# Performance work log

Hardware: AMD Instinct MI355X
Metric: run time of the kernel (lower is better)

The kernel has to match this reference:

```python
import jax, jax.numpy as jnp
import numpy as np
from jax import lax

DIM = 1024
H = 16          # num_heads
HD = DIM // H   # head dim (qk and v identical)
D_INNER = 4     # fast-weight inner dim
CHUNK = 16
BASE_LR = 1e-3
KSZ = 4         # short conv kernel size


def short_conv(x, w):
    # x: (b, l, c), w: (c, KSZ). Depthwise causal conv + residual (as in ShortConvolution).
    xT = jnp.transpose(x, (0, 2, 1))  # (b, c, l)
    y = lax.conv_general_dilated(xT, w[:, None, :], window_strides=(1,),
                                 padding=[(KSZ - 1, 0)], feature_group_count=x.shape[-1],
                                 dimension_numbers=('NCH', 'OIH', 'NCH'))
    return jnp.transpose(y + xT, (0, 2, 1))


def l2norm(x):
    # interpret torch.norm(..., dim=-1) as L2 normalization over head dim (required for shape consistency)
    return x / jnp.linalg.norm(x, axis=-1, keepdims=True)


def attn(q, k, v):
    # flash_attn_func equivalent: non-causal softmax attention, scale 1/sqrt(d)
    # q: (b, D, h, d), k/v: (b, L, h, d)
    s = jnp.einsum('bqhd,bkhd->bhqk', q, k) / jnp.sqrt(jnp.asarray(q.shape[-1], q.dtype))
    p = jax.nn.softmax(s, axis=-1)
    return jnp.einsum('bhqk,bkhd->bqhd', p, v)


def setup_inputs() -> dict:
    key = jax.random.key(0)
    ks = jax.random.split(key, 12)
    b, l = 4, 4096
    s = 1.0 / np.sqrt(DIM)
    return {
        'hidden_states': jax.random.normal(ks[0], (b, l, DIM), jnp.float32),
        'Wq': jax.random.normal(ks[1], (DIM, DIM), jnp.float32) * s,
        'Wk': jax.random.normal(ks[2], (DIM, DIM), jnp.float32) * s,
        'Wv': jax.random.normal(ks[3], (DIM, DIM), jnp.float32) * s,
        'Wlr': jax.random.normal(ks[4], (H * 2, DIM), jnp.float32) * s,
        'Wg': jax.random.normal(ks[5], (DIM, DIM), jnp.float32) * s,
        'Wo': jax.random.normal(ks[6], (DIM, DIM), jnp.float32) * s,
        'cq': jax.random.normal(ks[7], (DIM, KSZ), jnp.float32) * 0.1,
        'ck': jax.random.normal(ks[8], (DIM, KSZ), jnp.float32) * 0.1,
        'cv': jax.random.normal(ks[9], (DIM, KSZ), jnp.float32) * 0.1,
        'W_in_init': jax.random.normal(ks[10], (1, D_INNER, H, HD), jnp.float32) / np.sqrt(HD),
        'W_out_init': jax.random.normal(ks[11], (1, D_INNER, H, HD), jnp.float32) / np.sqrt(D_INNER),
        'ln_g': jnp.ones((HD,), jnp.float32),
        'ln_b': jnp.zeros((HD,), jnp.float32),
    }


def _forward(hidden_states, Wq, Wk, Wv, Wlr, Wg, Wo, cq, ck, cv, W_in_init, W_out_init, ln_g, ln_b):
    b, l, _ = hidden_states.shape
    q = l2norm(jax.nn.silu(short_conv(hidden_states @ Wq.T, cq)).reshape(b, l, H, HD))
    k = l2norm(jax.nn.silu(short_conv(hidden_states @ Wk.T, ck)).reshape(b, l, H, HD))
    v = jax.nn.silu(short_conv(hidden_states @ Wv.T, cv)).reshape(b, l, H, HD)
    lr = jax.nn.softplus(hidden_states @ Wlr.T + BASE_LR).reshape(b, l, H, 2)

    nc = l // CHUNK
    to_chunks = lambda x: x.reshape(b, nc, CHUNK, H, -1).transpose(1, 0, 2, 3, 4)
    qc, kc, vc, lrc = map(to_chunks, (q, k, v, lr))

    W_in0 = jnp.broadcast_to(W_in_init, (b, D_INNER, H, HD))
    W_out0 = jnp.broadcast_to(W_out_init, (b, D_INNER, H, HD))
    mask = jnp.tril(jnp.ones((CHUNK, CHUNK), jnp.float32))  # causal within chunk (diag kept)

    def step(carry, xs):
        W_in, W_out = carry
        q_t, k_t, v_t, lr_t = xs  # (b, CHUNK, H, d) / lr (b, CHUNK, H, 2)
        k_h = jax.nn.softmax(jnp.einsum('blhd,bDhd->blhD', k_t, W_in), axis=-1) * lr_t[..., 1:]
        q_h = jax.nn.softmax(jnp.einsum('blhd,bDhd->blhD', q_t, W_in), axis=-1)
        qk = jnp.einsum('bqhD,bkhD->bhqk', q_h, k_h) * mask
        o_t = jnp.einsum('bqhD,bDhd->bqhd', q_h, W_out) + jnp.einsum('bhqk,bkhd->bqhd', qk, v_t)
        W_out = W_out + jnp.einsum('bnhD,bnhd->bDhd', k_h, v_t)
        lr_in = lr_t[:, :1, :, 0:1]    # (b,1,h,1)
        lr_out = lr_t[:, :1, :, 1:2]
        # two nested test-time gradient steps via attention
        for _ in range(2):
            g_out = -attn(W_in, k_t, v_t)
            g_in = -attn(W_out, v_t, k_t)
            W_in = W_in - lr_in * g_in
            W_out = W_out - lr_out * g_out
        return (W_in, W_out), o_t

    _, o = lax.scan(step, (W_in0, W_out0), (qc, kc, vc, lrc))
    o = o.transpose(1, 0, 2, 3, 4).reshape(b, l, H, HD)

    mu = o.mean(-1, keepdims=True)
    var = ((o - mu) ** 2).mean(-1, keepdims=True)
    o = (o - mu) / jnp.sqrt(var + 1e-5) * ln_g + ln_b
    o = o.reshape(b, l, DIM)
    gate = hidden_states @ Wg.T
    return (o * gate) @ Wo.T


def reference(hidden_states, Wq, Wk, Wv, Wlr, Wg, Wo, cq, ck, cv, W_in_init, W_out_init, ln_g, ln_b):
    return _forward(hidden_states, Wq, Wk, Wv, Wlr, Wg, Wo, cq, ck, cv, W_in_init, W_out_init, ln_g, ln_b)
```

## Files before the change

kernel.cpp:

```cpp
#include <hip/hip_runtime.h>
#include <cstdint>
#include <cstddef>

#define DIM    1024
#define NH     16
#define HD     64
#define CHUNK_ 16
#define SEQ    4096
#define BATCH  4
#define NROWS  (BATCH * SEQ)
#define NCHUNK (SEQ / CHUNK_)
#define SEG    64
#define NSEG   (SEQ / SEG)

using bf16x8 = __attribute__((ext_vector_type(8))) short;
using f32x4  = __attribute__((ext_vector_type(4))) float;
typedef union { bf16x8 v; uint32_t u[4]; } B8;

#define MFMA16(a, b, c) __builtin_amdgcn_mfma_f32_16x16x32_bf16((a), (b), (c), 0, 0, 0)

__device__ __forceinline__ ushort f2bf(float f) {
    uint32_t u = __float_as_uint(f);
    u += 0x7FFFu + ((u >> 16) & 1u);
    return (ushort)(u >> 16);
}
__device__ __forceinline__ uint32_t pack2(float a, float b) {
    return (uint32_t)f2bf(a) | ((uint32_t)f2bf(b) << 16);
}
__device__ __forceinline__ float dot4(const float4 a, const float4 b) {
    return a.x*b.x + a.y*b.y + a.z*b.z + a.w*b.w;
}
__device__ __forceinline__ float redsum16(float x) {
    x += __shfl_xor(x, 1); x += __shfl_xor(x, 2);
    x += __shfl_xor(x, 4); x += __shfl_xor(x, 8);
    return x;
}

#define SYNC() do { asm volatile("" ::: "memory");          \
                    __builtin_amdgcn_wave_barrier();        \
                    __builtin_amdgcn_sched_barrier(0); } while (0)

__global__ __launch_bounds__(256)
void gemm_nt_bf16(const float* __restrict__ A, const float* __restrict__ B,
                  float* __restrict__ C, int K, int ldc)
{
    __shared__ ushort As[128][64];
    __shared__ ushort Bs[128][64];

    const int tid  = threadIdx.x;
    const int m0   = blockIdx.y * 128, n0 = blockIdx.x * 128;
    const int wave = tid >> 6, lane = tid & 63;
    const int wm   = (wave >> 1) * 64, wn = (wave & 1) * 64;
    const int frow = lane & 15, fkg = lane >> 4;
    const int srow = tid >> 1, shalf = tid & 1;

    f32x4 acc[4][4];
#pragma unroll
    for (int i = 0; i < 4; ++i)
#pragma unroll
        for (int j = 0; j < 4; ++j) acc[i][j] = (f32x4){0.f, 0.f, 0.f, 0.f};

    const float* Ap0 = A + (size_t)(m0 + srow) * K + shalf * 16;
    const float* Bp0 = B + (size_t)(n0 + srow) * K + shalf * 16;
    const int swz0 = ((shalf * 2 + 0) ^ (srow & 7)) * 8;
    const int swz1 = ((shalf * 2 + 1) ^ (srow & 7)) * 8;
    const int rsw  = (frow & 7);

    for (int kt = 0; kt < K; kt += 32) {
        float4 a0 = *(const float4*)(Ap0 + kt);
        float4 a1 = *(const float4*)(Ap0 + kt + 4);
        float4 a2 = *(const float4*)(Ap0 + kt + 8);
        float4 a3 = *(const float4*)(Ap0 + kt + 12);
        float4 b0 = *(const float4*)(Bp0 + kt);
        float4 b1 = *(const float4*)(Bp0 + kt + 4);
        float4 b2 = *(const float4*)(Bp0 + kt + 8);
        float4 b3 = *(const float4*)(Bp0 + kt + 12);

        __syncthreads();
        uint4 u;
        u.x = pack2(a0.x, a0.y); u.y = pack2(a0.z, a0.w);
        u.z = pack2(a1.x, a1.y); u.w = pack2(a1.z, a1.w);
        *(uint4*)&As[srow][swz0] = u;
        u.x = pack2(a2.x, a2.y); u.y = pack2(a2.z, a2.w);
        u.z = pack2(a3.x, a3.y); u.w = pack2(a3.z, a3.w);
        *(uint4*)&As[srow][swz1] = u;
        u.x = pack2(b0.x, b0.y); u.y = pack2(b0.z, b0.w);
        u.z = pack2(b1.x, b1.y); u.w = pack2(b1.z, b1.w);
        *(uint4*)&Bs[srow][swz0] = u;
        u.x = pack2(b2.x, b2.y); u.y = pack2(b2.z, b2.w);
        u.z = pack2(b3.x, b3.y); u.w = pack2(b3.z, b3.w);
        *(uint4*)&Bs[srow][swz1] = u;
        __syncthreads();

        bf16x8 af[4], bf[4];
#pragma unroll
        for (int i = 0; i < 4; ++i) {
            af[i] = *(const bf16x8*)&As[wm + i * 16 + frow][(fkg ^ rsw) * 8];
            bf[i] = *(const bf16x8*)&Bs[wn + i * 16 + frow][(fkg ^ rsw) * 8];
        }
#pragma unroll
        for (int mt = 0; mt < 4; ++mt)
#pragma unroll
            for (int nt = 0; nt < 4; ++nt)
                acc[mt][nt] = MFMA16(af[mt], bf[nt], acc[mt][nt]);
    }

    const int col = lane & 15, r4 = (lane >> 4) * 4;
#pragma unroll
    for (int mt = 0; mt < 4; ++mt)
#pragma unroll
        for (int nt = 0; nt < 4; ++nt)
#pragma unroll
            for (int j = 0; j < 4; ++j)
                C[(size_t)(m0 + wm + mt * 16 + r4 + j) * ldc +
                  (n0 + wn + nt * 16 + col)] = acc[mt][nt][j];
}

__global__ __launch_bounds__(256)
void lr_kernel(const float* __restrict__ hs, const float* __restrict__ Wlr,
               float* __restrict__ LR)
{
    __shared__ float row[DIM];
    const int r = blockIdx.x;
    const int t = threadIdx.x;
    *(float4*)&row[t * 4] = *(const float4*)&hs[(size_t)r * DIM + t * 4];
    __syncthreads();

    const int o = t >> 3;
    const int p = t & 7;
    const float* w = Wlr + (size_t)o * DIM + p * 128;
    const float* x = row + p * 128;
    float acc = 0.f;
#pragma unroll
    for (int i = 0; i < 32; ++i) {
        float4 xv = *(const float4*)(x + i * 4);
        float4 wv = *(const float4*)(w + i * 4);
        acc += dot4(xv, wv);
    }
    acc += __shfl_xor(acc, 1);
    acc += __shfl_xor(acc, 2);
    acc += __shfl_xor(acc, 4);
    if (p == 0) {
        float xx = acc + 0.001f;
        LR[(size_t)r * 32 + o] = (xx > 20.f) ? xx : log1pf(expf(xx));
    }
}

__global__ __launch_bounds__(256)
void halo_save(const float* __restrict__ Q, const float* __restrict__ K,
               const float* __restrict__ V, float* __restrict__ HALO)
{
    int idx = blockIdx.x;
    int tn  = idx / (BATCH * (NSEG - 1) * 3);
    int rem = idx - tn * (BATCH * (NSEG - 1) * 3);
    int b   = rem / ((NSEG - 1) * 3);
    int rem2= rem - b * ((NSEG - 1) * 3);
    int s   = rem2 / 3 + 1;
    int j   = rem2 - (s - 1) * 3;

    const float* buf = (tn == 0) ? Q : ((tn == 1) ? K : V);
    size_t src = ((size_t)(b * SEQ + s * SEG - 3 + j)) * DIM + threadIdx.x * 4;
    size_t dst = ((size_t)((tn * BATCH + b) * NSEG + s) * 3 + j) * DIM + threadIdx.x * 4;
    *(float4*)&HALO[dst] = *(const float4*)&buf[src];
}

__global__ __launch_bounds__(256)
void conv_inplace(float* __restrict__ Q, float* __restrict__ K,
                  float* __restrict__ V, const float* __restrict__ HALO,
                  const float* __restrict__ cq, const float* __restrict__ ck,
                  const float* __restrict__ cv)
{
    const int wid  = (blockIdx.x << 2) + (threadIdx.x >> 6);
    const int lane = threadIdx.x & 63;
    const int tn   = wid >> 12;
    const int rem  = wid & 4095;
    const int b    = rem >> 10;
    const int rem2 = rem & 1023;
    const int h    = rem2 >> 6;
    const int s    = rem2 & 63;
    const int c    = (h << 6) + lane;

    float* buf = (tn == 0) ? Q : ((tn == 1) ? K : V);
    const float* cw = (tn == 0) ? cq : ((tn == 1) ? ck : cv);
    float4 w4 = *(const float4*)(cw + (c << 2));

    float xm3 = 0.f, xm2 = 0.f, xm1 = 0.f;
    if (s > 0) {
        size_t hb = ((size_t)((tn * BATCH + b) * NSEG + s) * 3) * DIM + c;
        xm3 = HALO[hb];
        xm2 = HALO[hb + DIM];
        xm1 = HALO[hb + 2 * DIM];
    }

    size_t base = ((size_t)(b * SEQ + s * SEG)) * DIM + c;
    float x_next = buf[base];
#pragma unroll 4
    for (int i = 0; i < SEG; ++i) {
        float x = x_next;
        if (i < SEG - 1) x_next = buf[base + (size_t)(i + 1) * DIM];
        float y = xm3 * w4.x + xm2 * w4.y + xm1 * w4.z + x * w4.w + x;
        y = y / (1.f + __expf(-y));
        if (tn < 2) {
            float n2 = y * y;
#pragma unroll
            for (int m = 1; m < 64; m <<= 1) n2 += __shfl_xor(n2, m);
            y *= rsqrtf(n2);
        }
        buf[base + (size_t)i * DIM] = y;
        xm3 = xm2; xm2 = xm1; xm1 = x;
    }
}

__global__ __launch_bounds__(64)
void scan_kernel(const float* QP, const float* __restrict__ KP,
                 const float* __restrict__ VP, const float* __restrict__ LRb,
                 const float* __restrict__ GATE,
                 const float* __restrict__ Wi0, const float* __restrict__ Wo0,
                 const float* __restrict__ lng, const float* __restrict__ lnb,
                 float* OB)
{
    const int bh = blockIdx.x, b = bh >> 4, h = bh & 15;
    const int t  = threadIdx.x, lo = t & 15, g = t >> 4;

    __shared__ ushort KA[16][72], QA[16][72], VA[16][72];
    __shared__ ushort KT[64][24];
    __shared__ ushort VT[64][40];
    __shared__ ushort WiA[16][72], WoA[16][72];
    __shared__ ushort QKT[16][32];
    __shared__ ushort P0s[16][32], P1s[16][32], KH[16][32];
    __shared__ float  sG[16][68];

    for (int i = t; i < 16 * 72; i += 64) { ((ushort*)WiA)[i] = 0; ((ushort*)WoA)[i] = 0; }
    for (int i = t; i < 64 * 24; i += 64) ((ushort*)KT)[i] = 0;
    for (int i = t; i < 64 * 40; i += 64) ((ushort*)VT)[i] = 0;
    for (int i = t; i < 16 * 32; i += 64) {
        ((ushort*)QKT)[i] = 0; ((ushort*)P0s)[i] = 0;
        ((ushort*)P1s)[i] = 0; ((ushort*)KH)[i]  = 0;
    }

    f32x4 wiC[4], woC[4];
#pragma unroll
    for (int n = 0; n < 4; ++n) { wiC[n] = (f32x4){0,0,0,0}; woC[n] = (f32x4){0,0,0,0}; }
    if (g == 0) {
#pragma unroll
        for (int n = 0; n < 4; ++n)
#pragma unroll
            for (int D = 0; D < 4; ++D) {
                float wi = Wi0[((size_t)D * NH + h) * HD + 16 * n + lo];
                float wo = Wo0[((size_t)D * NH + h) * HD + 16 * n + lo];
                wiC[n][D] = wi; woC[n][D] = wo;
                WiA[D][16 * n + lo] = f2bf(wi);
                WoA[D][16 * n + lo] = f2bf(wo);
                VT[16 * n + lo][16 + D] = f2bf(wo);
            }
    }
    SYNC();

    float lnGr[4], lnBr[4];
#pragma unroll
    for (int n = 0; n < 4; ++n) { lnGr[n] = lng[16 * n + lo]; lnBr[n] = lnb[16 * n + lo]; }

    const int rowb = b * SEQ;
    float4 pq[4], pk[4], pv[4], pg[4];
    float plr = 0.f;
    {
#pragma unroll
        for (int i = 0; i < 4; ++i) {
            size_t go = (size_t)(rowb + i * 4 + g) * DIM + h * 64 + 4 * lo;
            pq[i] = *(const float4*)&QP[go];
            pk[i] = *(const float4*)&KP[go];
            pv[i] = *(const float4*)&VP[go];
            pg[i] = *(const float4*)&GATE[go];
        }
        if (t < 32) plr = LRb[(size_t)(rowb + (t >> 1)) * 32 + h * 2 + (t & 1)];
    }

    const f32x4 z4 = (f32x4){0.f, 0.f, 0.f, 0.f};

    for (int c = 0; c < NCHUNK; ++c) {
        const int rb = rowb + c * CHUNK_;

#pragma unroll
        for (int i = 0; i < 4; ++i) {
            const int row = i * 4 + g;
            *(float4*)&sG[row][4 * lo] = pg[i];
            uint2 uq; uq.x = pack2(pq[i].x, pq[i].y); uq.y = pack2(pq[i].z, pq[i].w);
            *(uint2*)&QA[row][4 * lo] = uq;
            uint2 uk; uk.x = pack2(pk[i].x, pk[i].y); uk.y = pack2(pk[i].z, pk[i].w);
            *(uint2*)&KA[row][4 * lo] = uk;
            uint2 uv; uv.x = pack2(pv[i].x, pv[i].y); uv.y = pack2(pv[i].z, pv[i].w);
            *(uint2*)&VA[row][4 * lo] = uv;
            KT[4 * lo + 0][row] = (ushort)(uk.x & 0xFFFF);
            KT[4 * lo + 1][row] = (ushort)(uk.x >> 16);
            KT[4 * lo + 2][row] = (ushort)(uk.y & 0xFFFF);
            KT[4 * lo + 3][row] = (ushort)(uk.y >> 16);
            VT[4 * lo + 0][row] = (ushort)(uv.x & 0xFFFF);
            VT[4 * lo + 1][row] = (ushort)(uv.x >> 16);
            VT[4 * lo + 2][row] = (ushort)(uv.y & 0xFFFF);
            VT[4 * lo + 3][row] = (ushort)(uv.y >> 16);
        }
        const float lr1    = __shfl(plr, 2 * lo + 1);
        const float lr_in  = __shfl(plr, 0);
        const float lr_out = __shfl(plr, 1);

        if (c + 1 < NCHUNK) {
            const int rb2 = rb + CHUNK_;
#pragma unroll
            for (int i = 0; i < 4; ++i) {
                size_t go = (size_t)(rb2 + i * 4 + g) * DIM + h * 64 + 4 * lo;
                pq[i] = *(const float4*)&QP[go];
                pk[i] = *(const float4*)&KP[go];
                pv[i] = *(const float4*)&VP[go];
                pg[i] = *(const float4*)&GATE[go];
            }
            if (t < 32) plr = LRb[(size_t)(rb2 + (t >> 1)) * 32 + h * 2 + (t & 1)];
        }
        SYNC();

        bf16x8 xWi0 = *(const bf16x8*)&WiA[lo][g * 8];
        bf16x8 xWi1 = *(const bf16x8*)&WiA[lo][g * 8 + 32];
        f32x4 cK = MFMA16(xWi0, *(const bf16x8*)&KA[lo][g * 8], z4);
        cK = MFMA16(xWi1, *(const bf16x8*)&KA[lo][g * 8 + 32], cK);
        f32x4 cQ = MFMA16(xWi0, *(const bf16x8*)&QA[lo][g * 8], z4);
        cQ = MFMA16(xWi1, *(const bf16x8*)&QA[lo][g * 8 + 32], cQ);

        float mK = fmaxf(fmaxf(cK[0], cK[1]), fmaxf(cK[2], cK[3]));
        float ek0 = __expf(cK[0] - mK), ek1 = __expf(cK[1] - mK);
        float ek2 = __expf(cK[2] - mK), ek3 = __expf(cK[3] - mK);
        float ivk = lr1 / (ek0 + ek1 + ek2 + ek3);
        float kh0 = ek0 * ivk, kh1 = ek1 * ivk, kh2 = ek2 * ivk, kh3 = ek3 * ivk;

        float mQ = fmaxf(fmaxf(cQ[0], cQ[1]), fmaxf(cQ[2], cQ[3]));
        float eq0 = __expf(cQ[0] - mQ), eq1 = __expf(cQ[1] - mQ);
        float eq2 = __expf(cQ[2] - mQ), eq3 = __expf(cQ[3] - mQ);
        float ivq = 1.f / (eq0 + eq1 + eq2 + eq3);
        float qh0 = eq0 * ivq, qh1 = eq1 * ivq, qh2 = eq2 * ivq, qh3 = eq3 * ivq;

        B8 aQh, bKh;
        aQh.u[0] = aQh.u[1] = aQh.u[2] = aQh.u[3] = 0;
        bKh.u[0] = bKh.u[1] = bKh.u[2] = bKh.u[3] = 0;
        if (g == 0) {
            aQh.u[0] = pack2(qh0, qh1); aQh.u[1] = pack2(qh2, qh3);
            bKh.u[0] = pack2(kh0, kh1); bKh.u[1] = pack2(kh2, kh3);
        }
        f32x4 cQK = MFMA16(aQh.v, bKh.v, z4);

#pragma unroll
        for (int r = 0; r < 4; ++r) {
            const int q = 4 * g + r;
            QKT[q][lo] = (lo <= q) ? f2bf(cQK[r]) : (ushort)0;
        }
        if (g == 0) {
            QKT[lo][16] = f2bf(qh0); QKT[lo][17] = f2bf(qh1);
            QKT[lo][18] = f2bf(qh2); QKT[lo][19] = f2bf(qh3);
            KH[0][lo] = f2bf(kh0); KH[1][lo] = f2bf(kh1);
            KH[2][lo] = f2bf(kh2); KH[3][lo] = f2bf(kh3);
        }
        SYNC();

        bf16x8 aO = *(const bf16x8*)&QKT[lo][g * 8];
        f32x4 oA[4];
#pragma unroll
        for (int n = 0; n < 4; ++n)
            oA[n] = MFMA16(aO, *(const bf16x8*)&VT[16 * n + lo][g * 8], z4);
#pragma unroll
        for (int r = 0; r < 4; ++r) {
            float s1 = oA[0][r] + oA[1][r] + oA[2][r] + oA[3][r];
            float s2 = oA[0][r] * oA[0][r] + oA[1][r] * oA[1][r] +
                       oA[2][r] * oA[2][r] + oA[3][r] * oA[3][r];
            s1 = redsum16(s1); s2 = redsum16(s2);
            float mu = s1 * (1.f / 64.f);
            float rstd = rsqrtf(s2 * (1.f / 64.f) - mu * mu + 1e-5f);
            const int q = 4 * g + r;
#pragma unroll
            for (int n = 0; n < 4; ++n) {
                float val = (oA[n][r] - mu) * rstd * lnGr[n] + lnBr[n];
                val *= sG[q][16 * n + lo];
                OB[(size_t)(rb + q) * DIM + h * 64 + 16 * n + lo] = val;
            }
        }

        {
            bf16x8 aKH = *(const bf16x8*)&KH[lo][g * 8];
#pragma unroll
            for (int n = 0; n < 4; ++n)
                woC[n] = MFMA16(aKH, *(const bf16x8*)&VT[16 * n + lo][g * 8], woC[n]);
        }
        if (g == 0) {
#pragma unroll
            for (int n = 0; n < 4; ++n)
#pragma unroll
                for (int D = 0; D < 4; ++D)
                    WoA[D][16 * n + lo] = f2bf(woC[n][D]);
        }
        SYNC();

#pragma unroll
        for (int it = 0; it < 2; ++it) {
            bf16x8 aK0 = *(const bf16x8*)&KA[lo][g * 8];
            bf16x8 aK1 = *(const bf16x8*)&KA[lo][g * 8 + 32];
            bf16x8 aV0 = *(const bf16x8*)&VA[lo][g * 8];
            bf16x8 aV1 = *(const bf16x8*)&VA[lo][g * 8 + 32];
            bf16x8 bWi0 = *(const bf16x8*)&WiA[lo][g * 8];
            bf16x8 bWi1 = *(const bf16x8*)&WiA[lo][g * 8 + 32];
            bf16x8 bWo0 = *(const bf16x8*)&WoA[lo][g * 8];
            bf16x8 bWo1 = *(const bf16x8*)&WoA[lo][g * 8 + 32];
            f32x4 s0T = MFMA16(aK0, bWi0, z4);
            s0T = MFMA16(aK1, bWi1, s0T);
            f32x4 s1T = MFMA16(aV0, bWo0, z4);
            s1T = MFMA16(aV1, bWo1, s1T);

            float x0[4], x1[4];
#pragma unroll
            for (int r = 0; r < 4; ++r) {
                x0[r] = s0T[r] * 0.125f;
                x1[r] = s1T[r] * 0.125f;
            }
            float m0 = fmaxf(fmaxf(x0[0], x0[1]), fmaxf(x0[2], x0[3]));
            float m1 = fmaxf(fmaxf(x1[0], x1[1]), fmaxf(x1[2], x1[3]));
            m0 = fmaxf(m0, __shfl_xor(m0, 16)); m0 = fmaxf(m0, __shfl_xor(m0, 32));
            m1 = fmaxf(m1, __shfl_xor(m1, 16)); m1 = fmaxf(m1, __shfl_xor(m1, 32));
            float e0[4], e1[4];
#pragma unroll
            for (int r = 0; r < 4; ++r) {
                e0[r] = __expf(x0[r] - m0);
                e1[r] = __expf(x1[r] - m1);
            }
            float su0 = e0[0] + e0[1] + e0[2] + e0[3];
            float su1 = e1[0] + e1[1] + e1[2] + e1[3];
            su0 += __shfl_xor(su0, 16); su0 += __shfl_xor(su0, 32);
            su1 += __shfl_xor(su1, 16); su1 += __shfl_xor(su1, 32);
            const float w0 = lr_out / su0;
            const float w1 = lr_in / su1;
            if (lo < 4) {
#pragma unroll
                for (int r = 0; r < 4; ++r) {
                    P0s[lo][4 * g + r] = f2bf(e0[r] * w0);
                    P1s[lo][4 * g + r] = f2bf(e1[r] * w1);
                }
            }
            SYNC();

            bf16x8 aP0 = *(const bf16x8*)&P0s[lo][g * 8];
            bf16x8 aP1 = *(const bf16x8*)&P1s[lo][g * 8];
#pragma unroll
            for (int n = 0; n < 4; ++n) {
                woC[n] = MFMA16(aP0, *(const bf16x8*)&VT[16 * n + lo][g * 8], woC[n]);
                wiC[n] = MFMA16(aP1, *(const bf16x8*)&KT[16 * n + lo][g * 8], wiC[n]);
            }
            if (g == 0) {
#pragma unroll
                for (int n = 0; n < 4; ++n)
#pragma unroll
                    for (int D = 0; D < 4; ++D) {
                        WiA[D][16 * n + lo] = f2bf(wiC[n][D]);
                        WoA[D][16 * n + lo] = f2bf(woC[n][D]);
                        if (it == 1) VT[16 * n + lo][16 + D] = f2bf(woC[n][D]);
                    }
            }
            SYNC();
        }
    }
}

extern "C" void kernel_launch(void* const* d_in, const int* in_sizes, int n_in,
                              void* d_out, int out_size, void* d_ws, size_t ws_size,
                              hipStream_t stream)
{
    const float* hs  = (const float*)d_in[0];
    const float* Wq  = (const float*)d_in[1];
    const float* Wk  = (const float*)d_in[2];
    const float* Wv  = (const float*)d_in[3];
    const float* Wlr = (const float*)d_in[4];
    const float* Wg  = (const float*)d_in[5];
    const float* Wo  = (const float*)d_in[6];
    const float* cq  = (const float*)d_in[7];
    const float* ck  = (const float*)d_in[8];
    const float* cv  = (const float*)d_in[9];
    const float* Wi0 = (const float*)d_in[10];
    const float* Wo0 = (const float*)d_in[11];
    const float* lng = (const float*)d_in[12];
    const float* lnb = (const float*)d_in[13];

    float* ws   = (float*)d_ws;
    float* Q    = ws;
    float* K    = Q + (size_t)NROWS * DIM;
    float* V    = K + (size_t)NROWS * DIM;
    float* LRb  = V + (size_t)NROWS * DIM;
    float* HALO = LRb + (size_t)NROWS * 32;
    float* GATE = (float*)d_out;
    float* OBUF = Q;

    dim3 blk(256);

    gemm_nt_bf16<<<dim3(8, 128), blk, 0, stream>>>(hs, Wq, Q,    1024, DIM);
    gemm_nt_bf16<<<dim3(8, 128), blk, 0, stream>>>(hs, Wk, K,    1024, DIM);
    gemm_nt_bf16<<<dim3(8, 128), blk, 0, stream>>>(hs, Wv, V,    1024, DIM);
    gemm_nt_bf16<<<dim3(8, 128), blk, 0, stream>>>(hs, Wg, GATE, 1024, DIM);

    lr_kernel<<<NROWS, blk, 0, stream>>>(hs, Wlr, LRb);

    halo_save<<<3 * BATCH * (NSEG - 1) * 3, blk, 0, stream>>>(Q, K, V, HALO);
    conv_inplace<<<(3 * BATCH * NH * NSEG) / 4, blk, 0, stream>>>(Q, K, V, HALO,
                                                                  cq, ck, cv);

    scan_kernel<<<BATCH * NH, dim3(64), 0, stream>>>(Q, K, V, LRb, GATE,
                                                     Wi0, Wo0, lng, lnb, OBUF);

    gemm_nt_bf16<<<dim3(8, 128), blk, 0, stream>>>(OBUF, Wo, (float*)d_out,
                                                   1024, 1024);
}
```

Before: 2.132 ms.

## Build softmax MFMA operands via shuffles, use DPP reductions, drop LR shuffles

The P0/P1 probability matrices are now repacked from MFMA accumulator layout into A-operand layout with cross-lane shuffles, instead of a round trip through shared memory plus a wave barrier. Each pass of the inner gradient loop loses one LDS write/read and one sync, at the cost of eight extra shuffles. The LayerNorm row reductions switch from shfl_xor to DPP row-rotate adds. Learning-rate values are loaded straight into registers in every lane rather than being broadcast by shuffles, which adds a few redundant global loads.

Result: faster. 2.051 ms (-3.8%).

```diff
diff --git a/kernel.cpp b/kernel.cpp
--- a/kernel.cpp
+++ b/kernel.cpp
@@ -30,9 +30,15 @@
 __device__ __forceinline__ float dot4(const float4 a, const float4 b) {
     return a.x*b.x + a.y*b.y + a.z*b.z + a.w*b.w;
 }
-__device__ __forceinline__ float redsum16(float x) {
-    x += __shfl_xor(x, 1); x += __shfl_xor(x, 2);
-    x += __shfl_xor(x, 4); x += __shfl_xor(x, 8);
+
+template <int N>
+__device__ __forceinline__ float ror16(float x) {
+    return __int_as_float(__builtin_amdgcn_update_dpp(
+        0, __float_as_int(x), 0x120 + N, 0xF, 0xF, true));
+}
+__device__ __forceinline__ float dppsum16(float x) {
+    x += ror16<1>(x); x += ror16<2>(x);
+    x += ror16<4>(x); x += ror16<8>(x);
     return x;
 }
 
@@ -227,16 +233,13 @@
     __shared__ ushort VT[64][40];
     __shared__ ushort WiA[16][72], WoA[16][72];
     __shared__ ushort QKT[16][32];
-    __shared__ ushort P0s[16][32], P1s[16][32], KH[16][32];
+    __shared__ ushort KH[16][32];
     __shared__ float  sG[16][68];
 
     for (int i = t; i < 16 * 72; i += 64) { ((ushort*)WiA)[i] = 0; ((ushort*)WoA)[i] = 0; }
     for (int i = t; i < 64 * 24; i += 64) ((ushort*)KT)[i] = 0;
     for (int i = t; i < 64 * 40; i += 64) ((ushort*)VT)[i] = 0;
-    for (int i = t; i < 16 * 32; i += 64) {
-        ((ushort*)QKT)[i] = 0; ((ushort*)P0s)[i] = 0;
-        ((ushort*)P1s)[i] = 0; ((ushort*)KH)[i]  = 0;
-    }
+    for (int i = t; i < 16 * 32; i += 64) { ((ushort*)QKT)[i] = 0; ((ushort*)KH)[i] = 0; }
 
     f32x4 wiC[4], woC[4];
 #pragma unroll
@@ -262,7 +265,7 @@
 
     const int rowb = b * SEQ;
     float4 pq[4], pk[4], pv[4], pg[4];
-    float plr = 0.f;
+    float plr_q, plr_i, plr_o;
     {
 #pragma unroll
         for (int i = 0; i < 4; ++i) {
@@ -272,10 +275,14 @@
             pv[i] = *(const float4*)&VP[go];
             pg[i] = *(const float4*)&GATE[go];
         }
-        if (t < 32) plr = LRb[(size_t)(rowb + (t >> 1)) * 32 + h * 2 + (t & 1)];
+        plr_q = LRb[(size_t)(rowb + lo) * 32 + h * 2 + 1];
+        plr_i = LRb[(size_t)rowb * 32 + h * 2];
+        plr_o = LRb[(size_t)rowb * 32 + h * 2 + 1];
     }
 
     const f32x4 z4 = (f32x4){0.f, 0.f, 0.f, 0.f};
+    const uint32_t pmsk = (g < 2) ? 0xFFFFFFFFu : 0u;
+    const int L0 = (lo + 32 * g) & 63, L1 = (L0 + 16) & 63;
 
     for (int c = 0; c < NCHUNK; ++c) {
         const int rb = rowb + c * CHUNK_;
@@ -299,9 +306,9 @@
             VT[4 * lo + 2][row] = (ushort)(uv.y & 0xFFFF);
             VT[4 * lo + 3][row] = (ushort)(uv.y >> 16);
         }
-        const float lr1    = __shfl(plr, 2 * lo + 1);
-        const float lr_in  = __shfl(plr, 0);
-        const float lr_out = __shfl(plr, 1);
+        const float lr1    = plr_q;
+        const float lr_in  = plr_i;
+        const float lr_out = plr_o;
 
         if (c + 1 < NCHUNK) {
             const int rb2 = rb + CHUNK_;
@@ -313,7 +320,9 @@
                 pv[i] = *(const float4*)&VP[go];
                 pg[i] = *(const float4*)&GATE[go];
             }
-            if (t < 32) plr = LRb[(size_t)(rb2 + (t >> 1)) * 32 + h * 2 + (t & 1)];
+            plr_q = LRb[(size_t)(rb2 + lo) * 32 + h * 2 + 1];
+            plr_i = LRb[(size_t)rb2 * 32 + h * 2];
+            plr_o = LRb[(size_t)rb2 * 32 + h * 2 + 1];
         }
         SYNC();
 
@@ -368,7 +377,7 @@
             float s1 = oA[0][r] + oA[1][r] + oA[2][r] + oA[3][r];
             float s2 = oA[0][r] * oA[0][r] + oA[1][r] * oA[1][r] +
                        oA[2][r] * oA[2][r] + oA[3][r] * oA[3][r];
-            s1 = redsum16(s1); s2 = redsum16(s2);
+            s1 = dppsum16(s1); s2 = dppsum16(s2);
             float mu = s1 * (1.f / 64.f);
             float rstd = rsqrtf(s2 * (1.f / 64.f) - mu * mu + 1e-5f);
             const int q = 4 * g + r;
@@ -379,7 +388,6 @@
                 OB[(size_t)(rb + q) * DIM + h * 64 + 16 * n + lo] = val;
             }
         }
-
         {
             bf16x8 aKH = *(const bf16x8*)&KH[lo][g * 8];
 #pragma unroll
@@ -432,21 +440,25 @@
             su1 += __shfl_xor(su1, 16); su1 += __shfl_xor(su1, 32);
             const float w0 = lr_out / su0;
             const float w1 = lr_in / su1;
-            if (lo < 4) {
-#pragma unroll
-                for (int r = 0; r < 4; ++r) {
-                    P0s[lo][4 * g + r] = f2bf(e0[r] * w0);
-                    P1s[lo][4 * g + r] = f2bf(e1[r] * w1);
-                }
-            }
-            SYNC();
-
-            bf16x8 aP0 = *(const bf16x8*)&P0s[lo][g * 8];
-            bf16x8 aP1 = *(const bf16x8*)&P1s[lo][g * 8];
+
+            uint32_t p00 = pack2(e0[0] * w0, e0[1] * w0);
+            uint32_t p01 = pack2(e0[2] * w0, e0[3] * w0);
+            uint32_t p10 = pack2(e1[0] * w1, e1[1] * w1);
+            uint32_t p11 = pack2(e1[2] * w1, e1[3] * w1);
+            B8 aP0, aP1;
+            aP0.u[0] = (uint32_t)__shfl((int)p00, L0) & pmsk;
+            aP0.u[1] = (uint32_t)__shfl((int)p01, L0) & pmsk;
+            aP0.u[2] = (uint32_t)__shfl((int)p00, L1) & pmsk;
+            aP0.u[3] = (uint32_t)__shfl((int)p01, L1) & pmsk;
+            aP1.u[0] = (uint32_t)__shfl((int)p10, L0) & pmsk;
+            aP1.u[1] = (uint32_t)__shfl((int)p11, L0) & pmsk;
+            aP1.u[2] = (uint32_t)__shfl((int)p10, L1) & pmsk;
+            aP1.u[3] = (uint32_t)__shfl((int)p11, L1) & pmsk;
+
 #pragma unroll
             for (int n = 0; n < 4; ++n) {
-                woC[n] = MFMA16(aP0, *(const bf16x8*)&VT[16 * n + lo][g * 8], woC[n]);
-                wiC[n] = MFMA16(aP1, *(const bf16x8*)&KT[16 * n + lo][g * 8], wiC[n]);
+                woC[n] = MFMA16(aP0.v, *(const bf16x8*)&VT[16 * n + lo][g * 8], woC[n]);
+                wiC[n] = MFMA16(aP1.v, *(const bf16x8*)&KT[16 * n + lo][g * 8], wiC[n]);
             }
             if (g == 0) {
 #pragma unroll
```
